# Performance work log

Hardware: AMD Instinct MI355X
Metric: run time of the kernel (lower is better)

Reference implementation:

```python
import jax, jax.numpy as jnp
import numpy as np


def setup_inputs() -> dict:
    key = jax.random.key(0)
    k1, k2, k3, k4 = jax.random.split(key, 4)
    Q, S, L, F, H = 32, 25, 64, 256, 64
    qs = jax.random.normal(k1, (Q, L, F), dtype=jnp.float32)
    hs = jax.random.normal(k2, (S, L, F), dtype=jnp.float32)
    # nn.Linear(feature_size, hidden_size): weight [H, F], bias [H]
    W = jax.random.normal(k3, (H, F), dtype=jnp.float32) * (1.0 / np.sqrt(F))
    b = jax.random.normal(k4, (H,), dtype=jnp.float32) * 0.01
    return {"qs": qs, "hs": hs, "W": W, "b": b}


def reference(qs, hs, W, b):
    # Project once instead of materializing the repeated 5D tensors before Linear.
    # Wq: [Q, L, H], Wh: [S, L, H]
    Wq = jnp.einsum("qlf,hf->qlh", qs, W) + b
    Wh = jnp.einsum("slf,hf->slh", hs, W) + b
    # score[q,s,i,j] = sum_h tanh(Wq[q,i,h] * Wh[s,j,h])  -- non-decomposable,
    # so the broadcasted [Q,S,L,L,H] tanh is the faithful (and dominant) compute.
    scores = jnp.sum(
        jnp.tanh(Wq[:, None, :, None, :] * Wh[None, :, None, :, :]), axis=-1
    )  # [Q, S, L, L]
    att = jax.nn.softmax(scores, axis=3)  # softmax over support sequence dim j
    # weighted sum of support states: hs_rep[q,s,i,j,:] = hs[s,j,:]
    out = jnp.einsum("qsij,sjf->qsif", att, hs)  # [Q, S, L, F]
    return out
```

## Files before the change

### kernel.cpp

```cpp
#include <hip/hip_runtime.h>


#define NQ 32
#define NS 25
#define NL 64
#define NF 256
#define NH 64

#define K2LOG2E 2.8853900817779268f
#define C_LOG2E 1.4426950408889634f

typedef __attribute__((ext_vector_type(8))) short bf16x8;
typedef __attribute__((ext_vector_type(4))) float f32x4;

__device__ inline unsigned short f2bf(float x) {
    union { float f; unsigned int u; } v; v.f = x;
    unsigned int r = v.u + 0x7fffu + ((v.u >> 16) & 1u);
    return (unsigned short)(r >> 16);
}

#define WS 260
__global__ __launch_bounds__(256) void prep_kernel(
    const float* __restrict__ qs, const float* __restrict__ hs,
    const float* __restrict__ W, const float* __restrict__ b,
    float* __restrict__ Wqs, float* __restrict__ Whs,
    unsigned short* __restrict__ hsT)
{
    __shared__ float lds[64 * WS];
    const int t = threadIdx.x;
    const int bid = blockIdx.x;

    if (bid < 228) {
        const int r0 = bid * 16;
        const float4* W4 = (const float4*)W;
#pragma unroll
        for (int u = 0; u < 16; ++u) {
            int idx = t + 256 * u;
            int wr = idx >> 6, fq = idx & 63;
            *(float4*)&lds[wr * WS + 4 * fq] = W4[idx];
        }
        __syncthreads();

        const int h = t & 63;
        const int w = t >> 6;
        const float bias = b[h];

        const float4* xp[4];
        int rws[4];
#pragma unroll
        for (int k = 0; k < 4; ++k) {
            int r = __builtin_amdgcn_readfirstlane(r0 + w * 4 + k);
            rws[k] = r;
            xp[k] = (const float4*)((r < 2048) ? (qs + (size_t)r * NF)
                                               : (hs + (size_t)(r - 2048) * NF));
        }
        float acc[4] = {0.f, 0.f, 0.f, 0.f};
#pragma unroll 4
        for (int f4 = 0; f4 < 64; ++f4) {
            float4 wv = *(const float4*)&lds[h * WS + 4 * f4];
#pragma unroll
            for (int k = 0; k < 4; ++k) {
                float4 x = xp[k][f4];
                acc[k] += x.x * wv.x + x.y * wv.y + x.z * wv.z + x.w * wv.w;
            }
        }
#pragma unroll
        for (int k = 0; k < 4; ++k) {
            int r = rws[k];
            float v = acc[k] + bias;
            if (r < 2048) Wqs[(size_t)r * NH + h] = v * K2LOG2E;
            else          Whs[(size_t)(r - 2048) * NH + h] = v;
        }
    } else {
        const int b2 = bid - 228;
        const int s = b2 >> 2;
        const int f0 = (b2 & 3) * 64;
        unsigned short* T = (unsigned short*)lds;
        const float4* h4p = (const float4*)(hs + (size_t)s * NL * NF);
#pragma unroll
        for (int u = 0; u < 4; ++u) {
            int idx = t + 256 * u;
            int j = idx >> 4, fq = idx & 15;
            float4 v = h4p[j * 64 + (f0 >> 2) + fq];
            T[(4 * fq + 0) * 72 + j] = f2bf(v.x);
            T[(4 * fq + 1) * 72 + j] = f2bf(v.y);
            T[(4 * fq + 2) * 72 + j] = f2bf(v.z);
            T[(4 * fq + 3) * 72 + j] = f2bf(v.w);
        }
        __syncthreads();
#pragma unroll
        for (int u = 0; u < 2; ++u) {
            int idx = t + 256 * u;
            int fl = idx >> 3, jg = idx & 7;
            uint4 v = *(const uint4*)&T[fl * 72 + jg * 8];
            *(uint4*)&hsT[(size_t)(s * 256 + f0 + fl) * 64 + jg * 8] = v;
        }
    }
}

#define AS 68
#define B_OFF 2176
#define SCS 65
#define ATT_BYTE 8704
#define HST_BYTE 13312
#define SMEMF 7936

__global__ __launch_bounds__(256, 5) void attn_kernel(
    const float* __restrict__ Wqs, const float* __restrict__ Whs,
    const unsigned short* __restrict__ hsT, float* __restrict__ out)
{
    __shared__ float smem[SMEMF];
    const int t = threadIdx.x;
    const int bid = blockIdx.x;
    const int half = bid & 1;
    const int s = (bid >> 1) % NS;
    const int q = bid / (2 * NS);

    {
        const float4* a4 = (const float4*)(Wqs + ((size_t)q * NL + half * 32) * NH);
        const float4* b4 = (const float4*)(Whs + (size_t)s * NL * NH);
#pragma unroll
        for (int u = 0; u < 2; ++u) {
            int idx = t + 256 * u;
            int i = idx >> 4, g = idx & 15;
            *(float4*)&smem[i * AS + 4 * g] = a4[idx];
        }
#pragma unroll
        for (int u = 0; u < 4; ++u) {
            int idx = t + 256 * u;
            int j = idx >> 4, g = idx & 15;
            *(float4*)&smem[B_OFF + j * AS + 4 * g] = b4[idx];
        }
    }
    __syncthreads();

    const int i0 = (t >> 4) * 2;
    const int jn = t & 15;
    float sum[2][4] = {{0.f, 0.f, 0.f, 0.f}, {0.f, 0.f, 0.f, 0.f}};

#pragma unroll 2
    for (int h4 = 0; h4 < 16; ++h4) {
        float4 av[2], bv[4];
        av[0] = *(const float4*)&smem[i0 * AS + 4 * h4];
        av[1] = *(const float4*)&smem[(i0 + 1) * AS + 4 * h4];
#pragma unroll
        for (int jj = 0; jj < 4; ++jj)
            bv[jj] = *(const float4*)&smem[B_OFF + (jn + 16 * jj) * AS + 4 * h4];
#pragma unroll
        for (int ii = 0; ii < 2; ++ii) {
#pragma unroll
            for (int jj = 0; jj < 4; ++jj) {
                float e0 = __builtin_amdgcn_exp2f(fminf(av[ii].x * bv[jj].x, 18.f));
                float e1 = __builtin_amdgcn_exp2f(fminf(av[ii].y * bv[jj].y, 18.f));
                float e2 = __builtin_amdgcn_exp2f(fminf(av[ii].z * bv[jj].z, 18.f));
                float e3 = __builtin_amdgcn_exp2f(fminf(av[ii].w * bv[jj].w, 18.f));
                float s01 = e0 + e1, s23 = e2 + e3;
                float d01 = fmaf(e0, e1, s01) + 1.f;
                float d23 = fmaf(e2, e3, s23) + 1.f;
                float num = fmaf(s01 + 2.f, d23, (s23 + 2.f) * d01);
                sum[ii][jj] = fmaf(num, __builtin_amdgcn_rcpf(d01 * d23), sum[ii][jj]);
            }
        }
    }
    __syncthreads();

#pragma unroll
    for (int ii = 0; ii < 2; ++ii)
#pragma unroll
        for (int jj = 0; jj < 4; ++jj)
            smem[(i0 + ii) * SCS + jn + 16 * jj] = -2.f * sum[ii][jj];
    __syncthreads();

    {
        const int i = t >> 3, c = t & 7;
        const float* row = &smem[i * SCS + c * 8];
        float v[8];
        float m = -1e30f;
#pragma unroll
        for (int k = 0; k < 8; ++k) { v[k] = row[k]; m = fmaxf(m, v[k]); }
        m = fmaxf(m, __shfl_xor(m, 1));
        m = fmaxf(m, __shfl_xor(m, 2));
        m = fmaxf(m, __shfl_xor(m, 4));
        float d = 0.f;
#pragma unroll
        for (int k = 0; k < 8; ++k) {
            float p = __builtin_amdgcn_exp2f((v[k] - m) * C_LOG2E);
            v[k] = p; d += p;
        }
        d += __shfl_xor(d, 1);
        d += __shfl_xor(d, 2);
        d += __shfl_xor(d, 4);
        const float inv = __builtin_amdgcn_rcpf(d);
        unsigned int w0 = f2bf(v[0] * inv) | ((unsigned int)f2bf(v[1] * inv) << 16);
        unsigned int w1 = f2bf(v[2] * inv) | ((unsigned int)f2bf(v[3] * inv) << 16);
        unsigned int w2 = f2bf(v[4] * inv) | ((unsigned int)f2bf(v[5] * inv) << 16);
        unsigned int w3 = f2bf(v[6] * inv) | ((unsigned int)f2bf(v[7] * inv) << 16);
        *(uint4*)((char*)smem + ATT_BYTE + i * 144 + c * 16) = make_uint4(w0, w1, w2, w3);
    }
    __syncthreads();

    const int lane = t & 63;
    const int wv = t >> 6;
    const int m15 = lane & 15;
    const int quad = lane >> 4;

    bf16x8 afr[2][2];
#pragma unroll
    for (int m = 0; m < 2; ++m)
#pragma unroll
        for (int k = 0; k < 2; ++k)
            afr[m][k] = *(const bf16x8*)((const char*)smem + ATT_BYTE
                          + (m * 16 + m15) * 144 + k * 64 + quad * 16);

    const unsigned short* hsTs = hsT + (size_t)s * NF * NL;
    for (int ch = 0; ch < 2; ++ch) {
#pragma unroll
        for (int u = 0; u < 4; ++u) {
            int idx = t + 256 * u;
            int fl = idx >> 3, jg = idx & 7;
            uint4 vv = *(const uint4*)(hsTs + (size_t)(ch * 128 + fl) * 64 + jg * 8);
            *(uint4*)((char*)smem + HST_BYTE + fl * 144 + jg * 16) = vv;
        }
        __syncthreads();

        f32x4 acc[2][2];
#pragma unroll
        for (int m = 0; m < 2; ++m)
#pragma unroll
            for (int n = 0; n < 2; ++n)
                acc[m][n] = (f32x4){0.f, 0.f, 0.f, 0.f};

#pragma unroll
        for (int k = 0; k < 2; ++k) {
            bf16x8 bfr[2];
#pragma unroll
            for (int n = 0; n < 2; ++n)
                bfr[n] = *(const bf16x8*)((const char*)smem + HST_BYTE
                            + (wv * 32 + n * 16 + m15) * 144 + k * 64 + quad * 16);
#pragma unroll
            for (int m = 0; m < 2; ++m)
#pragma unroll
                for (int n = 0; n < 2; ++n)
                    acc[m][n] = __builtin_amdgcn_mfma_f32_16x16x32_bf16(
                        afr[m][k], bfr[n], acc[m][n], 0, 0, 0);
        }

        const size_t obase = ((size_t)(q * NS + s) * NL + half * 32) * NF + ch * 128;
#pragma unroll
        for (int m = 0; m < 2; ++m)
#pragma unroll
            for (int n = 0; n < 2; ++n)
#pragma unroll
                for (int r = 0; r < 4; ++r)
                    out[obase + (size_t)(m * 16 + quad * 4 + r) * NF
                        + wv * 32 + n * 16 + m15] = acc[m][n][r];
        __syncthreads();
    }
}

extern "C" void kernel_launch(void* const* d_in, const int* in_sizes, int n_in,
                              void* d_out, int out_size, void* d_ws, size_t ws_size,
                              hipStream_t stream) {
    const float* qs = (const float*)d_in[0];
    const float* hs = (const float*)d_in[1];
    const float* W  = (const float*)d_in[2];
    const float* b  = (const float*)d_in[3];
    float* out = (float*)d_out;

    float* Wqs = (float*)d_ws;
    float* Whs = Wqs + NQ * NL * NH;
    unsigned short* hsT = (unsigned short*)(Whs + NS * NL * NH);

    prep_kernel<<<328, 256, 0, stream>>>(qs, hs, W, b, Wqs, Whs, hsT);
    attn_kernel<<<NQ * NS * 2, 256, 0, stream>>>(Wqs, Whs, hsT, out);
}
```

Measured before the change: 128.7 us.

## Use split-bf16 MFMA for projection and read hsT fragments directly from global

The projection GEMM in the prep kernel moves from a scalar FP32 dot product over an LDS copy of W to bf16 MFMA. Each operand is split into hi and lo bf16 parts, and three MFMAs per tile recover near-FP32 accuracy, so the prep kernel needs half as many blocks and no large LDS staging. In the attention kernel the hsT staging through LDS and its two chunk loop with barriers is removed. B fragments are now loaded straight from global memory into registers and all 256 output columns are computed in one pass, which lowers LDS use so the occupancy hint rises from 5 to 6 blocks. The trade-offs are more scattered global loads in place of LDS reuse, more accumulator registers, and projection accuracy that now rests on the hi/lo split.

```diff
diff --git a/kernel.cpp b/kernel.cpp
--- a/kernel.cpp
+++ b/kernel.cpp
@@ -19,63 +19,75 @@
     return (unsigned short)(r >> 16);
 }
 
-#define WS 260
+__device__ inline void cvt_hilo(float4 a, float4 b, bf16x8* hi, bf16x8* lo) {
+    float x[8] = {a.x, a.y, a.z, a.w, b.x, b.y, b.z, b.w};
+    bf16x8 h8, l8;
+#pragma unroll
+    for (int i = 0; i < 8; ++i) {
+        union { float f; unsigned int u; } v; v.f = x[i];
+        unsigned short hh = (unsigned short)(v.u >> 16);
+        h8[i] = (short)hh;
+        union { unsigned int u; float f; } hf; hf.u = (unsigned int)hh << 16;
+        union { float f; unsigned int u; } rv; rv.f = x[i] - hf.f;
+        l8[i] = (short)(unsigned short)(rv.u >> 16);
+    }
+    *hi = h8; *lo = l8;
+}
+
+#define PROJ_BLOCKS 114
 __global__ __launch_bounds__(256) void prep_kernel(
     const float* __restrict__ qs, const float* __restrict__ hs,
     const float* __restrict__ W, const float* __restrict__ b,
     float* __restrict__ Wqs, float* __restrict__ Whs,
     unsigned short* __restrict__ hsT)
 {
-    __shared__ float lds[64 * WS];
+    __shared__ unsigned short T[64 * 72];
     const int t = threadIdx.x;
     const int bid = blockIdx.x;
 
-    if (bid < 228) {
-        const int r0 = bid * 16;
-        const float4* W4 = (const float4*)W;
-#pragma unroll
-        for (int u = 0; u < 16; ++u) {
-            int idx = t + 256 * u;
-            int wr = idx >> 6, fq = idx & 63;
-            *(float4*)&lds[wr * WS + 4 * fq] = W4[idx];
-        }
-        __syncthreads();
-
-        const int h = t & 63;
-        const int w = t >> 6;
-        const float bias = b[h];
-
-        const float4* xp[4];
-        int rws[4];
-#pragma unroll
-        for (int k = 0; k < 4; ++k) {
-            int r = __builtin_amdgcn_readfirstlane(r0 + w * 4 + k);
-            rws[k] = r;
-            xp[k] = (const float4*)((r < 2048) ? (qs + (size_t)r * NF)
-                                               : (hs + (size_t)(r - 2048) * NF));
-        }
-        float acc[4] = {0.f, 0.f, 0.f, 0.f};
-#pragma unroll 4
-        for (int f4 = 0; f4 < 64; ++f4) {
-            float4 wv = *(const float4*)&lds[h * WS + 4 * f4];
-#pragma unroll
-            for (int k = 0; k < 4; ++k) {
-                float4 x = xp[k][f4];
-                acc[k] += x.x * wv.x + x.y * wv.y + x.z * wv.z + x.w * wv.w;
+    if (bid < PROJ_BLOCKS) {
+        const int w = t >> 6, lane = t & 63;
+        const int m15 = lane & 15, quad = lane >> 4;
+        const int r0 = bid * 32 + (w & 1) * 16;
+        const int h0 = (w >> 1) * 32;
+        const bool is_q = (r0 < 2048);
+        const float* Xrow = is_q ? (qs + (size_t)(r0 + m15) * NF)
+                                 : (hs + (size_t)(r0 - 2048 + m15) * NF);
+        f32x4 acc[2] = {(f32x4){0.f,0.f,0.f,0.f}, (f32x4){0.f,0.f,0.f,0.f}};
+
+#pragma unroll 2
+        for (int kk = 0; kk < 8; ++kk) {
+            const int f0 = kk * 32 + quad * 8;
+            bf16x8 xhi, xlo;
+            cvt_hilo(*(const float4*)(Xrow + f0), *(const float4*)(Xrow + f0 + 4),
+                     &xhi, &xlo);
+#pragma unroll
+            for (int nt = 0; nt < 2; ++nt) {
+                const float* Wrow = W + (size_t)(h0 + nt * 16 + m15) * NF + f0;
+                bf16x8 whi, wlo;
+                cvt_hilo(*(const float4*)(Wrow), *(const float4*)(Wrow + 4),
+                         &whi, &wlo);
+                acc[nt] = __builtin_amdgcn_mfma_f32_16x16x32_bf16(xhi, whi, acc[nt], 0, 0, 0);
+                acc[nt] = __builtin_amdgcn_mfma_f32_16x16x32_bf16(xhi, wlo, acc[nt], 0, 0, 0);
+                acc[nt] = __builtin_amdgcn_mfma_f32_16x16x32_bf16(xlo, whi, acc[nt], 0, 0, 0);
             }
         }
 #pragma unroll
-        for (int k = 0; k < 4; ++k) {
-            int r = rws[k];
-            float v = acc[k] + bias;
-            if (r < 2048) Wqs[(size_t)r * NH + h] = v * K2LOG2E;
-            else          Whs[(size_t)(r - 2048) * NH + h] = v;
+        for (int nt = 0; nt < 2; ++nt) {
+            const int h = h0 + nt * 16 + m15;
+            const float bias = b[h];
+#pragma unroll
+            for (int r = 0; r < 4; ++r) {
+                const int row = r0 + quad * 4 + r;
+                const float v = acc[nt][r] + bias;
+                if (is_q) Wqs[(size_t)row * NH + h] = v * K2LOG2E;
+                else      Whs[(size_t)(row - 2048) * NH + h] = v;
+            }
         }
     } else {
-        const int b2 = bid - 228;
+        const int b2 = bid - PROJ_BLOCKS;
         const int s = b2 >> 2;
         const int f0 = (b2 & 3) * 64;
-        unsigned short* T = (unsigned short*)lds;
         const float4* h4p = (const float4*)(hs + (size_t)s * NL * NF);
 #pragma unroll
         for (int u = 0; u < 4; ++u) {
@@ -102,10 +114,9 @@
 #define B_OFF 2176
 #define SCS 65
 #define ATT_BYTE 8704
-#define HST_BYTE 13312
-#define SMEMF 7936
-
-__global__ __launch_bounds__(256, 5) void attn_kernel(
+#define SMEMF 6528
+
+__global__ __launch_bounds__(256, 6) void attn_kernel(
     const float* __restrict__ Wqs, const float* __restrict__ Whs,
     const unsigned short* __restrict__ hsT, float* __restrict__ out)
 {
@@ -213,49 +224,36 @@
                           + (m * 16 + m15) * 144 + k * 64 + quad * 16);
 
     const unsigned short* hsTs = hsT + (size_t)s * NF * NL;
-    for (int ch = 0; ch < 2; ++ch) {
-#pragma unroll
-        for (int u = 0; u < 4; ++u) {
-            int idx = t + 256 * u;
-            int fl = idx >> 3, jg = idx & 7;
-            uint4 vv = *(const uint4*)(hsTs + (size_t)(ch * 128 + fl) * 64 + jg * 8);
-            *(uint4*)((char*)smem + HST_BYTE + fl * 144 + jg * 16) = vv;
-        }
-        __syncthreads();
-
-        f32x4 acc[2][2];
+    f32x4 acc[2][4];
+#pragma unroll
+    for (int m = 0; m < 2; ++m)
+#pragma unroll
+        for (int n = 0; n < 4; ++n) acc[m][n] = (f32x4){0.f, 0.f, 0.f, 0.f};
+
+#pragma unroll
+    for (int k = 0; k < 2; ++k) {
+        bf16x8 bfr[4];
+#pragma unroll
+        for (int n = 0; n < 4; ++n)
+            bfr[n] = *(const bf16x8*)(hsTs
+                        + (size_t)((wv * 4 + n) * 16 + m15) * 64 + k * 32 + quad * 8);
 #pragma unroll
         for (int m = 0; m < 2; ++m)
 #pragma unroll
-            for (int n = 0; n < 2; ++n)
-                acc[m][n] = (f32x4){0.f, 0.f, 0.f, 0.f};
-
-#pragma unroll
-        for (int k = 0; k < 2; ++k) {
-            bf16x8 bfr[2];
-#pragma unroll
-            for (int n = 0; n < 2; ++n)
-                bfr[n] = *(const bf16x8*)((const char*)smem + HST_BYTE
-                            + (wv * 32 + n * 16 + m15) * 144 + k * 64 + quad * 16);
-#pragma unroll
-            for (int m = 0; m < 2; ++m)
-#pragma unroll
-                for (int n = 0; n < 2; ++n)
-                    acc[m][n] = __builtin_amdgcn_mfma_f32_16x16x32_bf16(
-                        afr[m][k], bfr[n], acc[m][n], 0, 0, 0);
-        }
-
-        const size_t obase = ((size_t)(q * NS + s) * NL + half * 32) * NF + ch * 128;
-#pragma unroll
-        for (int m = 0; m < 2; ++m)
-#pragma unroll
-            for (int n = 0; n < 2; ++n)
-#pragma unroll
-                for (int r = 0; r < 4; ++r)
-                    out[obase + (size_t)(m * 16 + quad * 4 + r) * NF
-                        + wv * 32 + n * 16 + m15] = acc[m][n][r];
-        __syncthreads();
-    }
+            for (int n = 0; n < 4; ++n)
+                acc[m][n] = __builtin_amdgcn_mfma_f32_16x16x32_bf16(
+                    afr[m][k], bfr[n], acc[m][n], 0, 0, 0);
+    }
+
+    const size_t obase = ((size_t)(q * NS + s) * NL + half * 32) * NF;
+#pragma unroll
+    for (int m = 0; m < 2; ++m)
+#pragma unroll
+        for (int n = 0; n < 4; ++n)
+#pragma unroll
+            for (int r = 0; r < 4; ++r)
+                out[obase + (size_t)(m * 16 + quad * 4 + r) * NF
+                    + (wv * 4 + n) * 16 + m15] = acc[m][n][r];
 }
 
 extern "C" void kernel_launch(void* const* d_in, const int* in_sizes, int n_in,
@@ -271,6 +269,6 @@
     float* Whs = Wqs + NQ * NL * NH;
     unsigned short* hsT = (unsigned short*)(Whs + NS * NL * NH);
 
-    prep_kernel<<<328, 256, 0, stream>>>(qs, hs, W, b, Wqs, Whs, hsT);
+    prep_kernel<<<PROJ_BLOCKS + NS * 4, 256, 0, stream>>>(qs, hs, W, b, Wqs, Whs, hsT);
     attn_kernel<<<NQ * NS * 2, 256, 0, stream>>>(Wqs, Whs, hsT, out);
 }
```

After: 122.6 us. 4.8% less time.
